# Kernel tuning notes

Measured on AMD Instinct MI355X. Metric: run time of the kernel, lower is better.

The kernel has to match this reference:

```python
import jax, jax.numpy as jnp
import numpy as np

N = 100000   # occupied voxels
C = 128      # input_dim
G = 64       # voxel grid extent per axis


def _build_neighbor_map(rng):
    # random unique voxel coords in a G^3 grid + hash lookup for 3x3x3 offsets
    lin = rng.choice(G ** 3, size=N, replace=False)
    coords = np.stack(np.unravel_index(lin, (G, G, G)), axis=1).astype(np.int64)  # [N,3]
    lut = np.full(G ** 3, -1, np.int32)
    lut[lin] = np.arange(N, dtype=np.int32)
    o = np.arange(-1, 2)
    offs = np.stack(np.meshgrid(o, o, o, indexing='ij'), -1).reshape(27, 3)  # [27,3]
    nc = coords[None, :, :] + offs[:, None, :]                 # [27,N,3]
    valid = ((nc >= 0) & (nc < G)).all(-1)                     # [27,N]
    nlin = (nc[..., 0] * G + nc[..., 1]) * G + nc[..., 2]
    nbr = np.where(valid, lut[np.clip(nlin, 0, G ** 3 - 1)], -1).astype(np.int32)
    return nbr


def setup_inputs() -> dict:
    rng = np.random.default_rng(0)
    nbr = _build_neighbor_map(rng)
    key = jax.random.key(0)
    ks = jax.random.split(key, 5)
    h = C // 2
    x = jax.random.normal(ks[0], (N, C), jnp.float32)
    w1 = jax.random.normal(ks[1], (C, C), jnp.float32) * 0.05
    b1 = jnp.zeros((C,), jnp.float32)
    w2 = jax.random.normal(ks[2], (C, C), jnp.float32) * 0.05
    b2 = jnp.zeros((C,), jnp.float32)
    rw1 = jax.random.normal(ks[3], (27, h, h), jnp.float32) * 0.05
    rb1 = jnp.zeros((h,), jnp.float32)
    rw2 = jax.random.normal(ks[4], (27, h, h), jnp.float32) * 0.05
    rb2 = jnp.zeros((h,), jnp.float32)
    return dict(x=x, w1=w1, b1=b1, w2=w2, b2=b2,
                rw1=rw1, rb1=rb1, rw2=rw2, rb2=rb2,
                nbr=jnp.asarray(nbr))


def _sconv3(feat, nbr, W, b):
    # sparse 3x3x3 conv: gather neighbor features per kernel offset, GEMM, sum
    mask = (nbr >= 0).astype(feat.dtype)                  # [27,N]
    g = feat[jnp.maximum(nbr, 0)] * mask[:, :, None]      # [27,N,c]
    return jnp.einsum('knc,kcd->nd', g, W) + b            # [N,c]


def reference(x, w1, b1, w2, b2, rw1, rb1, rw2, rb2, nbr):
    h = x.shape[1] // 2
    y = x @ w1 + b1                                       # conv1 (1x1x1)
    conv_x, trans_x = y[:, :h], y[:, h:]                  # split
    # resblock (stride 1 -> no skip conv): relu(conv)->relu(conv) + identity
    r = jax.nn.relu(_sconv3(conv_x, nbr, rw1, rb1))
    r = jax.nn.relu(_sconv3(r, nbr, rw2, rb2))
    conv_x = (r + conv_x) + conv_x                        # resblock(x) + x
    # CodedVTRBlock source unavailable: modeled as identity on trans branch
    res = jnp.concatenate([conv_x, trans_x], axis=1) @ w2 + b2  # conv2 (1x1x1)
    return x + res
```

## Files before the change

kernel.cpp:

```cpp
#include <hip/hip_runtime.h>


#define N_PTS 100000
#define NBLK128 782
#define NBLK64 1563

typedef __attribute__((ext_vector_type(8))) short frag_ab;
typedef __attribute__((ext_vector_type(4))) float f32x4;
#define ZFRAG frag_ab{0, 0, 0, 0, 0, 0, 0, 0}

__device__ __forceinline__ unsigned short f2bf(float f) {
  union { float f; unsigned int i; } v; v.f = f;
  unsigned int r = v.i + 0x7fffu + ((v.i >> 16) & 1u);
  return (unsigned short)(r >> 16);
}
__device__ __forceinline__ float bf2f(unsigned short u) {
  union { unsigned int i; float f; } v; v.i = ((unsigned int)u) << 16; return v.f;
}

__device__ __forceinline__ void gload_lds16(const unsigned short* g, unsigned short* l) {
  __builtin_amdgcn_global_load_lds(
      (const __attribute__((address_space(1))) unsigned int*)g,
      (__attribute__((address_space(3))) unsigned int*)(unsigned int)(size_t)l,
      16, 0, 0);
}

__global__ __launch_bounds__(256) void k_prep(
    const float* __restrict__ w1, const float* __restrict__ w2,
    const float* __restrict__ rw1, const float* __restrict__ rw2,
    unsigned short* __restrict__ w1T, unsigned short* __restrict__ w2T,
    unsigned short* __restrict__ rw1T, unsigned short* __restrict__ rw2T) {
  int t = blockIdx.x * 256 + threadIdx.x;
  if (t < 128 * 128) {
    int c = t >> 7, d = t & 127;
    int pos = d * 128 + ((((c >> 3) ^ (d & 15)) << 3) | (c & 7));
    w1T[pos] = f2bf(w1[t]);
    w2T[pos] = f2bf(w2[t]);
  }
  if (t < 27 * 64 * 64) {
    int k = t >> 12, r = t & 4095, c = r >> 6, d = r & 63;
    int pos = (k << 12) + d * 64 + ((((c >> 3) ^ (d & 7)) << 3) | (c & 7));
    rw1T[pos] = f2bf(rw1[t]);
    rw2T[pos] = f2bf(rw2[t]);
  }
}

__global__ __launch_bounds__(256) void k_gemm_in(
    const float* __restrict__ x, const unsigned short* __restrict__ w1T,
    const float* __restrict__ b1, unsigned short* __restrict__ y) {
  __shared__ unsigned short sw[16384];
  const int tid = threadIdx.x, lane = tid & 63, w = tid >> 6;
  const int m16 = lane & 15, q = lane >> 4;
#pragma unroll
  for (int r = 0; r < 8; ++r) {
    const int off = (r * 256 + tid) * 8;
    gload_lds16(w1T + off, &sw[off]);
  }
  const int rowbase = blockIdx.x * 64 + w * 16;
  const int r0 = rowbase + m16;
  const int rc = r0 < N_PTS ? r0 : N_PTS - 1;
  float4 xr[4][2];
#pragma unroll
  for (int kk = 0; kk < 4; ++kk) {
    const float* xp = x + (size_t)rc * 128 + kk * 32 + q * 8;
    xr[kk][0] = *(const float4*)xp;
    xr[kk][1] = *(const float4*)(xp + 4);
  }
  __syncthreads();
  f32x4 acc[8] = {};
#pragma unroll
  for (int kk = 0; kk < 4; ++kk) {
    float4 f0 = xr[kk][0], f1 = xr[kk][1];
    frag_ab a;
    a[0] = (short)f2bf(f0.x); a[1] = (short)f2bf(f0.y);
    a[2] = (short)f2bf(f0.z); a[3] = (short)f2bf(f0.w);
    a[4] = (short)f2bf(f1.x); a[5] = (short)f2bf(f1.y);
    a[6] = (short)f2bf(f1.z); a[7] = (short)f2bf(f1.w);
#pragma unroll
    for (int ct = 0; ct < 8; ++ct) {
      const int d = ct * 16 + m16;
      const int phys = ((kk << 2) | q) ^ m16;
      frag_ab bf = *(const frag_ab*)(&sw[d * 128 + phys * 8]);
      acc[ct] = __builtin_amdgcn_mfma_f32_16x16x32_bf16(a, bf, acc[ct], 0, 0, 0);
    }
  }
#pragma unroll
  for (int ct = 0; ct < 8; ++ct) {
    const int col = ct * 16 + m16;
    const float bias = b1[col];
#pragma unroll
    for (int j = 0; j < 4; ++j) {
      int r = rowbase + q * 4 + j;
      if (r < N_PTS) y[(size_t)r * 128 + col] = f2bf(acc[ct][j] + bias);
    }
  }
}

template <bool FUSE>
__global__ __launch_bounds__(256) void k_conv(
    const unsigned short* __restrict__ feat, const int fstride,
    const int* __restrict__ nbr,
    const unsigned short* __restrict__ rwT, const float* __restrict__ rb,
    const unsigned short* __restrict__ res, unsigned short* __restrict__ out) {
  __shared__ unsigned short sw[2][4096];
  const int tid = threadIdx.x, lane = tid & 63, w = tid >> 6;
  const int m16 = lane & 15, q = lane >> 4;
  const int rowbase = blockIdx.x * 128 + w * 32;
  const int p0 = rowbase + m16, p1 = p0 + 16;
  const bool v0 = p0 < N_PTS, v1 = p1 < N_PTS;
  const int s0 = w * 1024 + lane * 8;
  const int s1 = s0 + 512;

  int i0r[2], i1r[2];
  i0r[0] = v0 ? nbr[p0] : -1;
  i1r[0] = v1 ? nbr[p1] : -1;
  i0r[1] = v0 ? nbr[N_PTS + p0] : -1;
  i1r[1] = v1 ? nbr[N_PTS + p1] : -1;

  frag_ab A[2][2][2];
#pragma unroll
  for (int a = 0; a < 2; ++a)
#pragma unroll
    for (int b = 0; b < 2; ++b)
#pragma unroll
      for (int c = 0; c < 2; ++c) A[a][b][c] = ZFRAG;

  {
    gload_lds16(rwT + s0, &sw[0][s0]);
    gload_lds16(rwT + s1, &sw[0][s1]);
    if (i0r[0] >= 0) {
      const unsigned short* fp = feat + (size_t)i0r[0] * fstride + q * 8;
      A[0][0][0] = *(const frag_ab*)fp; A[0][0][1] = *(const frag_ab*)(fp + 32);
    }
    if (i1r[0] >= 0) {
      const unsigned short* fp = feat + (size_t)i1r[0] * fstride + q * 8;
      A[0][1][0] = *(const frag_ab*)fp; A[0][1][1] = *(const frag_ab*)(fp + 32);
    }
  }
  __syncthreads();

  f32x4 acc[2][4] = {};
#pragma unroll
  for (int k = 0; k < 27; ++k) {
    const int b = k & 1;
    if (k + 1 < 27) {
      const unsigned short* src = rwT + ((k + 1) << 12);
      gload_lds16(src + s0, &sw[b ^ 1][s0]);
      gload_lds16(src + s1, &sw[b ^ 1][s1]);
      const int n = (k + 1) & 1;
      int j0 = i0r[n], j1 = i1r[n];
      A[n][0][0] = ZFRAG; A[n][0][1] = ZFRAG; A[n][1][0] = ZFRAG; A[n][1][1] = ZFRAG;
      if (j0 >= 0) {
        const unsigned short* fp = feat + (size_t)j0 * fstride + q * 8;
        A[n][0][0] = *(const frag_ab*)fp; A[n][0][1] = *(const frag_ab*)(fp + 32);
      }
      if (j1 >= 0) {
        const unsigned short* fp = feat + (size_t)j1 * fstride + q * 8;
        A[n][1][0] = *(const frag_ab*)fp; A[n][1][1] = *(const frag_ab*)(fp + 32);
      }
    }
    if (k + 2 < 27) {
      i0r[k & 1] = v0 ? nbr[(k + 2) * N_PTS + p0] : -1;
      i1r[k & 1] = v1 ? nbr[(k + 2) * N_PTS + p1] : -1;
    }
#pragma unroll
    for (int kk = 0; kk < 2; ++kk)
#pragma unroll
      for (int ct = 0; ct < 4; ++ct) {
        const int d = ct * 16 + m16;
        const int phys = ((kk << 2) | q) ^ (m16 & 7);
        frag_ab bf = *(const frag_ab*)(&sw[b][d * 64 + phys * 8]);
        acc[0][ct] = __builtin_amdgcn_mfma_f32_16x16x32_bf16(A[b][0][kk], bf, acc[0][ct], 0, 0, 0);
        acc[1][ct] = __builtin_amdgcn_mfma_f32_16x16x32_bf16(A[b][1][kk], bf, acc[1][ct], 0, 0, 0);
      }
    __syncthreads();
  }

#pragma unroll
  for (int ct = 0; ct < 4; ++ct) {
    const int col = ct * 16 + m16;
    const float bias = rb[col];
#pragma unroll
    for (int rt = 0; rt < 2; ++rt)
#pragma unroll
      for (int j = 0; j < 4; ++j) {
        const int r = rowbase + rt * 16 + q * 4 + j;
        if (r < N_PTS) {
          float v = acc[rt][ct][j] + bias;
          v = v > 0.f ? v : 0.f;
          if constexpr (FUSE) v += 2.f * bf2f(res[(size_t)r * 128 + col]);
          out[(size_t)r * 64 + col] = f2bf(v);
        }
      }
  }
}

__global__ __launch_bounds__(256) void k_gemm_out(
    const float* __restrict__ x, const unsigned short* __restrict__ z1,
    const unsigned short* __restrict__ y, const unsigned short* __restrict__ w2T,
    const float* __restrict__ b2, float* __restrict__ out) {
  __shared__ unsigned short sw[16384];
  const int tid = threadIdx.x, lane = tid & 63, w = tid >> 6;
  const int m16 = lane & 15, q = lane >> 4;
#pragma unroll
  for (int r = 0; r < 8; ++r) {
    const int off = (r * 256 + tid) * 8;
    gload_lds16(w2T + off, &sw[off]);
  }
  const int rowbase = blockIdx.x * 64 + w * 16;
  const int r0 = rowbase + m16;
  const int rc = r0 < N_PTS ? r0 : N_PTS - 1;
  frag_ab a[4];
#pragma unroll
  for (int kk = 0; kk < 4; ++kk) {
    const unsigned short* ap = (kk < 2)
        ? (z1 + (size_t)rc * 64 + kk * 32 + q * 8)
        : (y + (size_t)rc * 128 + 64 + (kk - 2) * 32 + q * 8);
    a[kk] = *(const frag_ab*)ap;
  }
  __syncthreads();
  f32x4 acc[8] = {};
#pragma unroll
  for (int kk = 0; kk < 4; ++kk)
#pragma unroll
    for (int ct = 0; ct < 8; ++ct) {
      const int d = ct * 16 + m16;
      const int phys = ((kk << 2) | q) ^ m16;
      frag_ab bf = *(const frag_ab*)(&sw[d * 128 + phys * 8]);
      acc[ct] = __builtin_amdgcn_mfma_f32_16x16x32_bf16(a[kk], bf, acc[ct], 0, 0, 0);
    }
#pragma unroll
  for (int ct = 0; ct < 8; ++ct) {
    const int col = ct * 16 + m16;
    const float bias = b2[col];
#pragma unroll
    for (int j = 0; j < 4; ++j) {
      int r = rowbase + q * 4 + j;
      if (r < N_PTS) {
        size_t o = (size_t)r * 128 + col;
        out[o] = acc[ct][j] + bias + x[o];
      }
    }
  }
}

extern "C" void kernel_launch(void* const* d_in, const int* in_sizes, int n_in,
                              void* d_out, int out_size, void* d_ws, size_t ws_size,
                              hipStream_t stream) {
  const float* x   = (const float*)d_in[0];
  const float* w1  = (const float*)d_in[1];
  const float* b1  = (const float*)d_in[2];
  const float* w2  = (const float*)d_in[3];
  const float* b2  = (const float*)d_in[4];
  const float* rw1 = (const float*)d_in[5];
  const float* rb1 = (const float*)d_in[6];
  const float* rw2 = (const float*)d_in[7];
  const float* rb2 = (const float*)d_in[8];
  const int* nbr = (const int*)d_in[9];
  float* out = (float*)d_out;

  char* ws = (char*)d_ws;
  unsigned short* w1T  = (unsigned short*)(ws);
  unsigned short* w2T  = (unsigned short*)(ws + 32768);
  unsigned short* rw1T = (unsigned short*)(ws + 65536);
  unsigned short* rw2T = (unsigned short*)(ws + 286720);
  unsigned short* y    = (unsigned short*)(ws + 507904);
  unsigned short* r1   = (unsigned short*)(ws + 507904 + 25600000);
  unsigned short* z1   = (unsigned short*)(ws + 507904 + 38400000);

  k_prep<<<432, 256, 0, stream>>>(w1, w2, rw1, rw2, w1T, w2T, rw1T, rw2T);
  k_gemm_in<<<NBLK64, 256, 0, stream>>>(x, w1T, b1, y);
  k_conv<false><<<NBLK128, 256, 0, stream>>>(y, 128, nbr, rw1T, rb1, nullptr, r1);
  k_conv<true><<<NBLK128, 256, 0, stream>>>(r1, 64, nbr, rw2T, rb2, y, z1);
  k_gemm_out<<<NBLK64, 256, 0, stream>>>(x, z1, y, w2T, b2, out);
}
```

Before: 245.2 us.

## Split y into compact conv/trans buffers, double rows per GEMM block, coalesce weight prep

The intermediate y is now written as two dense 64-column bf16 arrays (conv half and trans half) instead of one 128-wide array. This makes the gathered neighbor rows in the first sparse conv compact, with a 128-byte row stride, and makes the residual and trans reads contiguous. The two 1x1 GEMM kernels each process two 64-row chunks per block, so the LDS weight load is amortised over twice the work and the second chunk's loads overlap the first chunk's compute. Weight prep now transposes through LDS with vectorised 16-byte stores in 43 blocks instead of 432 scattered-store blocks. In exchange, the GEMM kernels use more registers and launch half as many blocks.

```diff
diff --git a/kernel.cpp b/kernel.cpp
--- a/kernel.cpp
+++ b/kernel.cpp
@@ -3,7 +3,6 @@
 
 #define N_PTS 100000
 #define NBLK128 782
-#define NBLK64 1563
 
 typedef __attribute__((ext_vector_type(8))) short frag_ab;
 typedef __attribute__((ext_vector_type(4))) float f32x4;
@@ -30,24 +29,56 @@
     const float* __restrict__ rw1, const float* __restrict__ rw2,
     unsigned short* __restrict__ w1T, unsigned short* __restrict__ w2T,
     unsigned short* __restrict__ rw1T, unsigned short* __restrict__ rw2T) {
-  int t = blockIdx.x * 256 + threadIdx.x;
-  if (t < 128 * 128) {
-    int c = t >> 7, d = t & 127;
-    int pos = d * 128 + ((((c >> 3) ^ (d & 15)) << 3) | (c & 7));
-    w1T[pos] = f2bf(w1[t]);
-    w2T[pos] = f2bf(w2[t]);
-  }
-  if (t < 27 * 64 * 64) {
-    int k = t >> 12, r = t & 4095, c = r >> 6, d = r & 63;
-    int pos = (k << 12) + d * 64 + ((((c >> 3) ^ (d & 7)) << 3) | (c & 7));
-    rw1T[pos] = f2bf(rw1[t]);
-    rw2T[pos] = f2bf(rw2[t]);
+  __shared__ unsigned short L[8320];
+  const int tid = threadIdx.x, bid = blockIdx.x;
+  if (bid < 16) {
+    const float* src = (bid < 8) ? w1 : w2;
+    unsigned short* dst = (bid < 8) ? w1T : w2T;
+    const int seg = bid & 7;
+#pragma unroll
+    for (int i = 0; i < 8; ++i) {
+      int idx = i * 256 + tid;
+      int c = idx >> 4, dl = idx & 15;
+      L[c * 17 + dl] = f2bf(src[c * 128 + seg * 16 + dl]);
+    }
+    __syncthreads();
+    const int dl = tid >> 4, j = tid & 15;
+    const int d = seg * 16 + dl;
+    frag_ab v;
+#pragma unroll
+    for (int i = 0; i < 8; ++i) v[i] = (short)L[(8 * j + i) * 17 + dl];
+    *(frag_ab*)(dst + d * 128 + ((j ^ (d & 15)) << 3)) = v;
+  } else {
+    const int k = bid - 16;
+#pragma unroll
+    for (int i = 0; i < 16; ++i) {
+      int idx = i * 256 + tid;
+      int c = idx >> 6, d = idx & 63;
+      L[c * 65 + d] = f2bf(rw1[k * 4096 + idx]);
+      L[4160 + c * 65 + d] = f2bf(rw2[k * 4096 + idx]);
+    }
+    __syncthreads();
+#pragma unroll
+    for (int h = 0; h < 2; ++h) {
+      int cid = h * 256 + tid;
+      int d = cid >> 3, j = cid & 7;
+      frag_ab v1, v2;
+#pragma unroll
+      for (int i = 0; i < 8; ++i) {
+        v1[i] = (short)L[(8 * j + i) * 65 + d];
+        v2[i] = (short)L[4160 + (8 * j + i) * 65 + d];
+      }
+      int pos = k * 4096 + d * 64 + ((j ^ (d & 7)) << 3);
+      *(frag_ab*)(rw1T + pos) = v1;
+      *(frag_ab*)(rw2T + pos) = v2;
+    }
   }
 }
 
 __global__ __launch_bounds__(256) void k_gemm_in(
     const float* __restrict__ x, const unsigned short* __restrict__ w1T,
-    const float* __restrict__ b1, unsigned short* __restrict__ y) {
+    const float* __restrict__ b1, unsigned short* __restrict__ yc,
+    unsigned short* __restrict__ yt) {
   __shared__ unsigned short sw[16384];
   const int tid = threadIdx.x, lane = tid & 63, w = tid >> 6;
   const int m16 = lane & 15, q = lane >> 4;
@@ -56,42 +87,92 @@
     const int off = (r * 256 + tid) * 8;
     gload_lds16(w1T + off, &sw[off]);
   }
-  const int rowbase = blockIdx.x * 64 + w * 16;
-  const int r0 = rowbase + m16;
-  const int rc = r0 < N_PTS ? r0 : N_PTS - 1;
-  float4 xr[4][2];
+  const int ci0 = blockIdx.x * 2;
+  const int rb0 = ci0 * 64 + w * 16;
+  const int rc0 = (rb0 + m16) < N_PTS ? (rb0 + m16) : N_PTS - 1;
+  float4 xA[4][2];
 #pragma unroll
   for (int kk = 0; kk < 4; ++kk) {
-    const float* xp = x + (size_t)rc * 128 + kk * 32 + q * 8;
-    xr[kk][0] = *(const float4*)xp;
-    xr[kk][1] = *(const float4*)(xp + 4);
+    const float* xp = x + (size_t)rc0 * 128 + kk * 32 + q * 8;
+    xA[kk][0] = *(const float4*)xp;
+    xA[kk][1] = *(const float4*)(xp + 4);
   }
   __syncthreads();
-  f32x4 acc[8] = {};
+
+  const int rb1 = (ci0 + 1) * 64 + w * 16;
+  const int rc1 = (rb1 + m16) < N_PTS ? (rb1 + m16) : N_PTS - 1;
+  float4 xB[4][2];
 #pragma unroll
   for (int kk = 0; kk < 4; ++kk) {
-    float4 f0 = xr[kk][0], f1 = xr[kk][1];
-    frag_ab a;
-    a[0] = (short)f2bf(f0.x); a[1] = (short)f2bf(f0.y);
-    a[2] = (short)f2bf(f0.z); a[3] = (short)f2bf(f0.w);
-    a[4] = (short)f2bf(f1.x); a[5] = (short)f2bf(f1.y);
-    a[6] = (short)f2bf(f1.z); a[7] = (short)f2bf(f1.w);
+    const float* xp = x + (size_t)rc1 * 128 + kk * 32 + q * 8;
+    xB[kk][0] = *(const float4*)xp;
+    xB[kk][1] = *(const float4*)(xp + 4);
+  }
+
+  {
+    f32x4 acc[8] = {};
+#pragma unroll
+    for (int kk = 0; kk < 4; ++kk) {
+      float4 f0 = xA[kk][0], f1 = xA[kk][1];
+      frag_ab a;
+      a[0] = (short)f2bf(f0.x); a[1] = (short)f2bf(f0.y);
+      a[2] = (short)f2bf(f0.z); a[3] = (short)f2bf(f0.w);
+      a[4] = (short)f2bf(f1.x); a[5] = (short)f2bf(f1.y);
+      a[6] = (short)f2bf(f1.z); a[7] = (short)f2bf(f1.w);
+#pragma unroll
+      for (int ct = 0; ct < 8; ++ct) {
+        const int d = ct * 16 + m16;
+        const int phys = ((kk << 2) | q) ^ m16;
+        frag_ab bf = *(const frag_ab*)(&sw[d * 128 + phys * 8]);
+        acc[ct] = __builtin_amdgcn_mfma_f32_16x16x32_bf16(a, bf, acc[ct], 0, 0, 0);
+      }
+    }
 #pragma unroll
     for (int ct = 0; ct < 8; ++ct) {
-      const int d = ct * 16 + m16;
-      const int phys = ((kk << 2) | q) ^ m16;
-      frag_ab bf = *(const frag_ab*)(&sw[d * 128 + phys * 8]);
-      acc[ct] = __builtin_amdgcn_mfma_f32_16x16x32_bf16(a, bf, acc[ct], 0, 0, 0);
-    }
-  }
-#pragma unroll
-  for (int ct = 0; ct < 8; ++ct) {
-    const int col = ct * 16 + m16;
-    const float bias = b1[col];
-#pragma unroll
-    for (int j = 0; j < 4; ++j) {
-      int r = rowbase + q * 4 + j;
-      if (r < N_PTS) y[(size_t)r * 128 + col] = f2bf(acc[ct][j] + bias);
+      const int col = ct * 16 + m16;
+      const float bias = b1[col];
+#pragma unroll
+      for (int j = 0; j < 4; ++j) {
+        int r = rb0 + q * 4 + j;
+        if (r < N_PTS) {
+          unsigned short val = f2bf(acc[ct][j] + bias);
+          if (ct < 4) yc[(size_t)r * 64 + col] = val;
+          else        yt[(size_t)r * 64 + (col - 64)] = val;
+        }
+      }
+    }
+  }
+  {
+    f32x4 acc[8] = {};
+#pragma unroll
+    for (int kk = 0; kk < 4; ++kk) {
+      float4 f0 = xB[kk][0], f1 = xB[kk][1];
+      frag_ab a;
+      a[0] = (short)f2bf(f0.x); a[1] = (short)f2bf(f0.y);
+      a[2] = (short)f2bf(f0.z); a[3] = (short)f2bf(f0.w);
+      a[4] = (short)f2bf(f1.x); a[5] = (short)f2bf(f1.y);
+      a[6] = (short)f2bf(f1.z); a[7] = (short)f2bf(f1.w);
+#pragma unroll
+      for (int ct = 0; ct < 8; ++ct) {
+        const int d = ct * 16 + m16;
+        const int phys = ((kk << 2) | q) ^ m16;
+        frag_ab bf = *(const frag_ab*)(&sw[d * 128 + phys * 8]);
+        acc[ct] = __builtin_amdgcn_mfma_f32_16x16x32_bf16(a, bf, acc[ct], 0, 0, 0);
+      }
+    }
+#pragma unroll
+    for (int ct = 0; ct < 8; ++ct) {
+      const int col = ct * 16 + m16;
+      const float bias = b1[col];
+#pragma unroll
+      for (int j = 0; j < 4; ++j) {
+        int r = rb1 + q * 4 + j;
+        if (r < N_PTS) {
+          unsigned short val = f2bf(acc[ct][j] + bias);
+          if (ct < 4) yc[(size_t)r * 64 + col] = val;
+          else        yt[(size_t)r * 64 + (col - 64)] = val;
+        }
+      }
     }
   }
 }
@@ -188,7 +269,7 @@
         if (r < N_PTS) {
           float v = acc[rt][ct][j] + bias;
           v = v > 0.f ? v : 0.f;
-          if constexpr (FUSE) v += 2.f * bf2f(res[(size_t)r * 128 + col]);
+          if constexpr (FUSE) v += 2.f * bf2f(res[(size_t)r * 64 + col]);
           out[(size_t)r * 64 + col] = f2bf(v);
         }
       }
@@ -197,7 +278,7 @@
 
 __global__ __launch_bounds__(256) void k_gemm_out(
     const float* __restrict__ x, const unsigned short* __restrict__ z1,
-    const unsigned short* __restrict__ y, const unsigned short* __restrict__ w2T,
+    const unsigned short* __restrict__ yt, const unsigned short* __restrict__ w2T,
     const float* __restrict__ b2, float* __restrict__ out) {
   __shared__ unsigned short sw[16384];
   const int tid = threadIdx.x, lane = tid & 63, w = tid >> 6;
@@ -207,38 +288,77 @@
     const int off = (r * 256 + tid) * 8;
     gload_lds16(w2T + off, &sw[off]);
   }
-  const int rowbase = blockIdx.x * 64 + w * 16;
-  const int r0 = rowbase + m16;
-  const int rc = r0 < N_PTS ? r0 : N_PTS - 1;
-  frag_ab a[4];
+  const int ci0 = blockIdx.x * 2;
+  const int rb0 = ci0 * 64 + w * 16;
+  const int rc0 = (rb0 + m16) < N_PTS ? (rb0 + m16) : N_PTS - 1;
+  frag_ab aA[4];
 #pragma unroll
   for (int kk = 0; kk < 4; ++kk) {
     const unsigned short* ap = (kk < 2)
-        ? (z1 + (size_t)rc * 64 + kk * 32 + q * 8)
-        : (y + (size_t)rc * 128 + 64 + (kk - 2) * 32 + q * 8);
-    a[kk] = *(const frag_ab*)ap;
+        ? (z1 + (size_t)rc0 * 64 + kk * 32 + q * 8)
+        : (yt + (size_t)rc0 * 64 + (kk - 2) * 32 + q * 8);
+    aA[kk] = *(const frag_ab*)ap;
   }
   __syncthreads();
-  f32x4 acc[8] = {};
-#pragma unroll
-  for (int kk = 0; kk < 4; ++kk)
+
+  const int rb1 = (ci0 + 1) * 64 + w * 16;
+  const int rc1 = (rb1 + m16) < N_PTS ? (rb1 + m16) : N_PTS - 1;
+  frag_ab aB[4];
+#pragma unroll
+  for (int kk = 0; kk < 4; ++kk) {
+    const unsigned short* ap = (kk < 2)
+        ? (z1 + (size_t)rc1 * 64 + kk * 32 + q * 8)
+        : (yt + (size_t)rc1 * 64 + (kk - 2) * 32 + q * 8);
+    aB[kk] = *(const frag_ab*)ap;
+  }
+
+  {
+    f32x4 acc[8] = {};
+#pragma unroll
+    for (int kk = 0; kk < 4; ++kk)
+#pragma unroll
+      for (int ct = 0; ct < 8; ++ct) {
+        const int d = ct * 16 + m16;
+        const int phys = ((kk << 2) | q) ^ m16;
+        frag_ab bf = *(const frag_ab*)(&sw[d * 128 + phys * 8]);
+        acc[ct] = __builtin_amdgcn_mfma_f32_16x16x32_bf16(aA[kk], bf, acc[ct], 0, 0, 0);
+      }
 #pragma unroll
     for (int ct = 0; ct < 8; ++ct) {
-      const int d = ct * 16 + m16;
-      const int phys = ((kk << 2) | q) ^ m16;
-      frag_ab bf = *(const frag_ab*)(&sw[d * 128 + phys * 8]);
-      acc[ct] = __builtin_amdgcn_mfma_f32_16x16x32_bf16(a[kk], bf, acc[ct], 0, 0, 0);
-    }
-#pragma unroll
-  for (int ct = 0; ct < 8; ++ct) {
-    const int col = ct * 16 + m16;
-    const float bias = b2[col];
-#pragma unroll
-    for (int j = 0; j < 4; ++j) {
-      int r = rowbase + q * 4 + j;
-      if (r < N_PTS) {
-        size_t o = (size_t)r * 128 + col;
-        out[o] = acc[ct][j] + bias + x[o];
+      const int col = ct * 16 + m16;
+      const float bias = b2[col];
+#pragma unroll
+      for (int j = 0; j < 4; ++j) {
+        int r = rb0 + q * 4 + j;
+        if (r < N_PTS) {
+          size_t o = (size_t)r * 128 + col;
+          out[o] = acc[ct][j] + bias + x[o];
+        }
+      }
+    }
+  }
+  {
+    f32x4 acc[8] = {};
+#pragma unroll
+    for (int kk = 0; kk < 4; ++kk)
+#pragma unroll
+      for (int ct = 0; ct < 8; ++ct) {
+        const int d = ct * 16 + m16;
+        const int phys = ((kk << 2) | q) ^ m16;
+        frag_ab bf = *(const frag_ab*)(&sw[d * 128 + phys * 8]);
+        acc[ct] = __builtin_amdgcn_mfma_f32_16x16x32_bf16(aB[kk], bf, acc[ct], 0, 0, 0);
+      }
+#pragma unroll
+    for (int ct = 0; ct < 8; ++ct) {
+      const int col = ct * 16 + m16;
+      const float bias = b2[col];
+#pragma unroll
+      for (int j = 0; j < 4; ++j) {
+        int r = rb1 + q * 4 + j;
+        if (r < N_PTS) {
+          size_t o = (size_t)r * 128 + col;
+          out[o] = acc[ct][j] + bias + x[o];
+        }
       }
     }
   }
@@ -264,13 +384,14 @@
   unsigned short* w2T  = (unsigned short*)(ws + 32768);
   unsigned short* rw1T = (unsigned short*)(ws + 65536);
   unsigned short* rw2T = (unsigned short*)(ws + 286720);
-  unsigned short* y    = (unsigned short*)(ws + 507904);
+  unsigned short* yc   = (unsigned short*)(ws + 507904);
+  unsigned short* yt   = (unsigned short*)(ws + 507904 + 12800000);
   unsigned short* r1   = (unsigned short*)(ws + 507904 + 25600000);
   unsigned short* z1   = (unsigned short*)(ws + 507904 + 38400000);
 
-  k_prep<<<432, 256, 0, stream>>>(w1, w2, rw1, rw2, w1T, w2T, rw1T, rw2T);
-  k_gemm_in<<<NBLK64, 256, 0, stream>>>(x, w1T, b1, y);
-  k_conv<false><<<NBLK128, 256, 0, stream>>>(y, 128, nbr, rw1T, rb1, nullptr, r1);
-  k_conv<true><<<NBLK128, 256, 0, stream>>>(r1, 64, nbr, rw2T, rb2, y, z1);
-  k_gemm_out<<<NBLK64, 256, 0, stream>>>(x, z1, y, w2T, b2, out);
-}
+  k_prep<<<43, 256, 0, stream>>>(w1, w2, rw1, rw2, w1T, w2T, rw1T, rw2T);
+  k_gemm_in<<<NBLK128, 256, 0, stream>>>(x, w1T, b1, yc, yt);
+  k_conv<false><<<NBLK128, 256, 0, stream>>>(yc, 64, nbr, rw1T, rb1, nullptr, r1);
+  k_conv<true><<<NBLK128, 256, 0, stream>>>(r1, 64, nbr, rw2T, rb2, yc, z1);
+  k_gemm_out<<<NBLK128, 256, 0, stream>>>(x, z1, yt, w2T, b2, out);
+}
```

Result: slower. 263.5 us (+7.5%).
